# Kernel tuning notes

Measured on AMD Instinct MI355X. Metric: run time of the kernel, lower is better.

The kernel has to match this reference:

```python
import jax, jax.numpy as jnp
import numpy as np

B, V, S, D, H, OBS = 8, 6, 32, 128, 128, 768
LN_EPS = 1e-5
KL_EPS = 1e-5


def setup_inputs() -> dict:
    key = jax.random.key(0)
    ks = jax.random.split(key, 32)
    n = lambda k, sh, s=1.0: jax.random.normal(k, sh, jnp.float32) * s
    w = 0.02  # param init scale
    inp = {
        'student_f0': n(ks[0], (B, V, 256, 32, 88)),
        'student_f1': n(ks[1], (B, V, 512, 16, 44)),
        'teacher_f0': n(ks[2], (B, V, 256, 32, 88)),
        'teacher_f1': n(ks[3], (B, V, 512, 16, 44)),
        'cam_mask': jax.random.randint(ks[4], (B, V), 0, 2).astype(bool),
        'eps_prior': n(ks[5], (V, B, S)),
        'eps_post': n(ks[6], (V, B, S)),
        # obs_encoder: Linear(768,128) -> LN -> SiLU -> Linear(128,128) -> SiLU
        'enc_w1': n(ks[7], (OBS, H), w), 'enc_b1': jnp.zeros((H,)),
        'ln_g': jnp.ones((H,)), 'ln_b': jnp.zeros((H,)),
        'enc_w2': n(ks[8], (H, H), w), 'enc_b2': jnp.zeros((H,)),
        # prior_net: Linear(128,128) -> SiLU -> Linear(128,64)
        'prior_w1': n(ks[9], (D, H), w), 'prior_b1': jnp.zeros((H,)),
        'prior_w2': n(ks[10], (H, 2 * S), w), 'prior_b2': jnp.zeros((2 * S,)),
        # post_net: Linear(128+128,128) -> SiLU -> Linear(128,64)
        'post_w1': n(ks[11], (D + H, H), w), 'post_b1': jnp.zeros((H,)),
        'post_w2': n(ks[12], (H, 2 * S), w), 'post_b2': jnp.zeros((2 * S,)),
        # decoder: Linear(128+32,128) -> SiLU -> Linear(128,768)
        'dec_w1': n(ks[13], (D + S, H), w), 'dec_b1': jnp.zeros((H,)),
        'dec_w2': n(ks[14], (H, OBS), w), 'dec_b2': jnp.zeros((OBS,)),
        # GRUCell(32 -> 128), torch gate order r,z,n
        'gru_wih': n(ks[15], (S, 3 * D), w), 'gru_whh': n(ks[16], (D, 3 * D), w),
        'gru_bih': jnp.zeros((3 * D,)), 'gru_bhh': jnp.zeros((3 * D,)),
    }
    return inp


def _layernorm(x, g, b):
    mu = x.mean(-1, keepdims=True)
    var = ((x - mu) ** 2).mean(-1, keepdims=True)
    return (x - mu) * jax.lax.rsqrt(var + LN_EPS) * g + b


def _rssm(obs, tgt, mask_f, eps_prior, eps_post, p):
    # obs/tgt: [V,B,OBS]; mask_f: [V,B]; eps: [V,B,S]
    silu = jax.nn.silu

    def step(carry, xs):
        deter, rl, rs, kl_acc, kn = carry
        obs_t, tgt_t, m_t, ep_pr, ep_po = xs
        # obs encoder
        h1 = silu(_layernorm(obs_t @ p['enc_w1'] + p['enc_b1'], p['ln_g'], p['ln_b']))
        obs_embed = silu(h1 @ p['enc_w2'] + p['enc_b2'])
        # prior / posterior stats
        pr = silu(deter @ p['prior_w1'] + p['prior_b1']) @ p['prior_w2'] + p['prior_b2']
        prior_mu, prior_lv = pr[..., :S], pr[..., S:]
        po_in = jnp.concatenate([deter, obs_embed], axis=-1)
        po = silu(po_in @ p['post_w1'] + p['post_b1']) @ p['post_w2'] + p['post_b2']
        post_mu, post_lv = po[..., :S], po[..., S:]
        # reparameterize both, select prior where camera is missing
        z_post = post_mu + ep_po * jnp.exp(0.5 * post_lv)
        z_prior = prior_mu + ep_pr * jnp.exp(0.5 * prior_lv)
        m = m_t[:, None]  # [B,1] float, 1 = use prior
        z = jnp.where(m > 0, z_prior, z_post)
        # GRUCell
        gi = z @ p['gru_wih'] + p['gru_bih']
        gh = deter @ p['gru_whh'] + p['gru_bhh']
        ir, iz, inn = jnp.split(gi, 3, axis=-1)
        hr, hz, hn = jnp.split(gh, 3, axis=-1)
        r = jax.nn.sigmoid(ir + hr)
        u = jax.nn.sigmoid(iz + hz)
        nn_ = jnp.tanh(inn + r * hn)
        deter = (1.0 - u) * nn_ + u * deter
        # decoder + losses
        decoded = silu(jnp.concatenate([deter, z], axis=-1) @ p['dec_w1'] + p['dec_b1']) @ p['dec_w2'] + p['dec_b2']
        recon = ((decoded - tgt_t) ** 2).mean(-1, keepdims=True)  # [B,1]
        miss_sum = m.sum()
        has_rec = miss_sum > 0
        rl = rl + jnp.where(has_rec, (recon * m).sum() / jnp.maximum(miss_sum, 1.0), 0.0)
        rs = rs + has_rec.astype(jnp.float32)
        var_q = jnp.maximum(jnp.exp(post_lv), KL_EPS)
        var_p = jnp.maximum(jnp.exp(prior_lv), KL_EPS)
        kl = 0.5 * ((var_q + (post_mu - prior_mu) ** 2) / var_p - 1.0 + prior_lv - post_lv)
        kl = kl.sum(-1, keepdims=True)  # [B,1]
        obs_m = 1.0 - m
        obs_sum = obs_m.sum()
        has_kl = obs_sum > 0
        kl_acc = kl_acc + jnp.where(has_kl, (kl * obs_m).sum() / jnp.maximum(obs_sum, 1.0), 0.0)
        kn = kn + has_kl.astype(jnp.float32)
        return (deter, rl, rs, kl_acc, kn), None

    init = (jnp.zeros((obs.shape[1], D), obs.dtype), 0.0, 0.0, 0.0, 0.0)
    (deter, rl, rs, kl_acc, kn), _ = jax.lax.scan(step, init, (obs, tgt, mask_f, eps_prior, eps_post))
    rec_loss = rl / jnp.maximum(rs, 1.0)
    kl_loss = kl_acc / jnp.maximum(kn, 1.0)
    return rec_loss, kl_loss


def reference(student_f0, student_f1, teacher_f0, teacher_f1, cam_mask, eps_prior, eps_post,
              enc_w1, enc_b1, ln_g, ln_b, enc_w2, enc_b2,
              prior_w1, prior_b1, prior_w2, prior_b2,
              post_w1, post_b1, post_w2, post_b2,
              dec_w1, dec_b1, dec_w2, dec_b2,
              gru_wih, gru_whh, gru_bih, gru_bhh):
    p = dict(enc_w1=enc_w1, enc_b1=enc_b1, ln_g=ln_g, ln_b=ln_b, enc_w2=enc_w2, enc_b2=enc_b2,
             prior_w1=prior_w1, prior_b1=prior_b1, prior_w2=prior_w2, prior_b2=prior_b2,
             post_w1=post_w1, post_b1=post_b1, post_w2=post_w2, post_b2=post_b2,
             dec_w1=dec_w1, dec_b1=dec_b1, dec_w2=dec_w2, dec_b2=dec_b2,
             gru_wih=gru_wih, gru_whh=gru_whh, gru_bih=gru_bih, gru_bhh=gru_bhh)
    # multi-scale spatial mean-pool then concat channels: [B,V,OBS]
    obs = jnp.concatenate([student_f0.mean((-1, -2)), student_f1.mean((-1, -2))], axis=-1)
    tgt = jax.lax.stop_gradient(
        jnp.concatenate([teacher_f0.mean((-1, -2)), teacher_f1.mean((-1, -2))], axis=-1))
    obs_T = jnp.transpose(obs, (1, 0, 2))   # [V,B,OBS]
    tgt_T = jnp.transpose(tgt, (1, 0, 2))
    mask_T = cam_mask.astype(jnp.float32).T  # [V,B]
    rec_loss, kl_loss = _rssm(obs_T, tgt_T, mask_T, eps_prior, eps_post, p)
    return jnp.stack([rec_loss * 1.0, kl_loss * 1e-4])  # [loss_world_rec, loss_world_kl]
```

## Files before the change

### kernel.cpp

```cpp
#include <hip/hip_runtime.h>
#include <cstddef>

constexpr int NB = 8;
constexpr int NV = 6;
constexpr int NS = 32;
constexpr int ND = 128;
constexpr int NH = 128;
constexpr int NOBS = 768;

constexpr int NJOBS = 18432;
constexpr int RWAVES = 8192;

typedef float vf4 __attribute__((ext_vector_type(4)));

__device__ __forceinline__ float sigf(float x) { return 1.0f / (1.0f + expf(-x)); }
__device__ __forceinline__ float siluf(float x) { return x / (1.0f + expf(-x)); }

__device__ __forceinline__ const vf4* lndr(const void* p) {
    asm volatile("" : "+s"(p));
    return (const vf4*)p;
}
#define PHASE_FENCE() do { __builtin_amdgcn_sched_barrier(0); asm volatile("" ::: "memory"); } while (0)

template<int NB8>
__device__ __forceinline__ vf4 dotk(const vf4* __restrict__ w, int ldg, int g, int k0,
                                    const float* __restrict__ x) {
    vf4 acc = {0.f, 0.f, 0.f, 0.f};
    vf4 wa[8], wb[8];
    #pragma unroll
    for (int i = 0; i < 8; i++) wa[i] = w[(size_t)(k0 + i) * ldg + g];
    #pragma unroll
    for (int bb = 0; bb < NB8; bb++) {
        int kb = k0 + bb * 8;
        if ((bb & 1) == 0) {
            if (bb + 1 < NB8) {
                #pragma unroll
                for (int i = 0; i < 8; i++) wb[i] = w[(size_t)(kb + 8 + i) * ldg + g];
            }
            #pragma unroll
            for (int i = 0; i < 8; i++) acc += x[kb + i] * wa[i];
        } else {
            if (bb + 1 < NB8) {
                #pragma unroll
                for (int i = 0; i < 8; i++) wa[i] = w[(size_t)(kb + 8 + i) * ldg + g];
            }
            #pragma unroll
            for (int i = 0; i < 8; i++) acc += x[kb + i] * wb[i];
        }
    }
    return acc;
}

__device__ __forceinline__ void reduce_job(int wid, int lane,
    const float* __restrict__ f0, const float* __restrict__ f1,
    float* __restrict__ out)
{
    if (wid < 12288) {
        const vf4* s4 = (const vf4*)(f0 + (size_t)wid * 2816);
        vf4 xb[11];
        #pragma unroll
        for (int it = 0; it < 11; it++) xb[it] = __builtin_nontemporal_load(&s4[lane + it * 64]);
        float s = 0.f;
        #pragma unroll
        for (int it = 0; it < 11; it++) s += xb[it].x + xb[it].y + xb[it].z + xb[it].w;
        #pragma unroll
        for (int o = 32; o > 0; o >>= 1) s += __shfl_down(s, o);
        if (lane == 0) {
            int b = wid / 1536, r = wid % 1536, v = r >> 8, c = r & 255;
            out[(size_t)(v * NB + b) * NOBS + c] = s * (1.0f / 2816.0f);
        }
    } else {
        int q = wid - 12288;
        int g = lane >> 4, sub = lane & 15;
        const vf4* s4 = (const vf4*)(f1 + (size_t)q * 2816);
        vf4 xb[11];
        #pragma unroll
        for (int it = 0; it < 11; it++) xb[it] = __builtin_nontemporal_load(&s4[g * 176 + sub + it * 16]);
        float s = 0.f;
        #pragma unroll
        for (int it = 0; it < 11; it++) s += xb[it].x + xb[it].y + xb[it].z + xb[it].w;
        #pragma unroll
        for (int o = 8; o > 0; o >>= 1) s += __shfl_down(s, o, 16);
        if (sub == 0) {
            int c4 = 4 * q + g;
            int b = c4 / 3072, r = c4 % 3072, v = r >> 9, c = r & 511;
            out[(size_t)(v * NB + b) * NOBS + 256 + c] = s * (1.0f / 704.0f);
        }
    }
}

__global__ __launch_bounds__(256) void reduce_obs(
    const float* __restrict__ sf0, const float* __restrict__ sf1,
    float* __restrict__ obs)
{
    int lane = threadIdx.x & 63;
    int w0 = blockIdx.x * 4 + (threadIdx.x >> 6);
    for (int wid = w0; wid < NJOBS; wid += RWAVES)
        reduce_job(wid, lane, sf0, sf1, obs);
}

__global__ __launch_bounds__(512) void encoder(
    const float* __restrict__ obs,
    const float* __restrict__ w1, const float* __restrict__ b1,
    const float* __restrict__ g, const float* __restrict__ be,
    const float* __restrict__ w2, const float* __restrict__ b2,
    float* __restrict__ obs_embed,
    const void* cam, float* __restrict__ maskf,
    const float* __restrict__ prior_w1, const float* __restrict__ post_w1,
    const float* __restrict__ prior_w2, const float* __restrict__ post_w2,
    const float* __restrict__ gru_wih,  const float* __restrict__ gru_whh,
    float* __restrict__ warm_dummy)
{
    int tid = threadIdx.x;

    if (blockIdx.x == 48) {
        if (tid != 0) return;
        const int* wi = (const int*)cam;
        bool is_i32 = true;
        for (int i = 0; i < NB * NV; i++) {
            unsigned v = (unsigned)wi[i];
            if (v > 1u) { is_i32 = false; break; }
        }
        const unsigned char* wb = (const unsigned char*)cam;
        for (int b = 0; b < NB; b++)
            for (int v = 0; v < NV; v++) {
                int val = is_i32 ? wi[b * NV + v] : (int)wb[b * NV + v];
                maskf[v * NB + b] = val ? 1.0f : 0.0f;
            }
        return;
    }
    if (blockIdx.x > 48) {
        int wtid = (blockIdx.x - 49) * 512 + tid;
        const float* arrs[6] = {prior_w1, post_w1, prior_w2, post_w2, gru_wih, gru_whh};
        const int n4s[6] = {4096, 8192, 2048, 2048, 3072, 12288};
        float s = 0.f;
        for (int a = 0; a < 6; a++) {
            const vf4* p = (const vf4*)arrs[a];
            int n4 = n4s[a];
            for (int i = wtid; i < n4; i += 16 * 512) {
                vf4 x = p[i];
                s += x.x + x.y + x.z + x.w;
            }
        }
        warm_dummy[wtid & 63] = s;
        return;
    }

    __shared__ float xs[NOBS];
    __shared__ float hs[NH];
    __shared__ float pE[4][NH];
    __shared__ float red[2], red2[2];
    int r = blockIdx.x;
    const float* row = obs + (size_t)r * NOBS;
    for (int i = tid; i < NOBS; i += 512) xs[i] = row[i];
    __syncthreads();

    {
        int part = tid >> 7, j = tid & 127;
        int k0 = part * 192;
        float a = 0.0f;
        #pragma unroll 8
        for (int k = k0; k < k0 + 192; k++) a += xs[k] * w1[k * NH + j];
        pE[part][j] = a;
    }
    __syncthreads();

    float a1 = 0.0f;
    if (tid < NH) {
        a1 = b1[tid] + pE[0][tid] + pE[1][tid] + pE[2][tid] + pE[3][tid];
        float v = a1;
        for (int o = 32; o > 0; o >>= 1) v += __shfl_down(v, o);
        if ((tid & 63) == 0) red[tid >> 6] = v;
    }
    __syncthreads();
    if (tid < NH) {
        float mu = (red[0] + red[1]) * (1.0f / 128.0f);
        float d = a1 - mu;
        float dv = d * d;
        for (int o = 32; o > 0; o >>= 1) dv += __shfl_down(dv, o);
        if ((tid & 63) == 0) red2[tid >> 6] = dv;
    }
    __syncthreads();
    if (tid < NH) {
        float mu = (red[0] + red[1]) * (1.0f / 128.0f);
        float var = (red2[0] + red2[1]) * (1.0f / 128.0f);
        float xn = (a1 - mu) * rsqrtf(var + 1e-5f) * g[tid] + be[tid];
        hs[tid] = siluf(xn);
    }
    __syncthreads();

    {
        int part = tid >> 7, j = tid & 127;
        int k0 = part * 32;
        float a = 0.0f;
        #pragma unroll 8
        for (int k = k0; k < k0 + 32; k++) a += hs[k] * w2[k * NH + j];
        pE[part][j] = a;
    }
    __syncthreads();
    if (tid < NH) {
        float a = b2[tid] + pE[0][tid] + pE[1][tid] + pE[2][tid] + pE[3][tid];
        obs_embed[(size_t)r * NH + tid] = siluf(a);
    }
}

__global__ __launch_bounds__(256) void fused_scan_tgt(
    const float* __restrict__ obs_embed,
    const float* __restrict__ maskf,
    const float* __restrict__ eps_prior, const float* __restrict__ eps_post,
    const float* __restrict__ prior_w1, const float* __restrict__ prior_b1,
    const float* __restrict__ prior_w2, const float* __restrict__ prior_b2,
    const float* __restrict__ post_w1, const float* __restrict__ post_b1,
    const float* __restrict__ post_w2, const float* __restrict__ post_b2,
    const float* __restrict__ gru_wih, const float* __restrict__ gru_whh,
    const float* __restrict__ gru_bih, const float* __restrict__ gru_bhh,
    float* __restrict__ deter_all, float* __restrict__ z_all,
    float* __restrict__ kl_out,
    const float* __restrict__ tf0, const float* __restrict__ tf1,
    float* __restrict__ tgt)
{
    __shared__ float pbuf[1024];
    __shared__ float gi_s[3 * ND];
    __shared__ float deter_obs[ND + NH];
    __shared__ float t12[2 * NH];
    __shared__ float pmu[NS], plv[NS], qmu[NS], qlv[NS], zsm[NS];
    vf4* pbuf4 = (vf4*)pbuf;
    float* deter = deter_obs;

    int tid = threadIdx.x;

    if (blockIdx.x >= 8) {
        int lane = tid & 63;
        int w0 = (blockIdx.x - 8) * 4 + (tid >> 6);
        for (int wid = w0; wid < NJOBS; wid += RWAVES)
            reduce_job(wid, lane, tf0, tf1, tgt);
        return;
    }

    int b = blockIdx.x;

    if (tid < ND) deter[tid] = 0.0f;
    __syncthreads();

    for (int t = 0; t < NV; t++) {
        const vf4* w_pw1  = lndr(prior_w1);
        const vf4* w_ow1  = lndr(post_w1);
        const vf4* w_pw2  = lndr(prior_w2);
        const vf4* w_ow2  = lndr(post_w2);
        const vf4* w_gih  = lndr(gru_wih);
        const vf4* w_ghh  = lndr(gru_whh);

        int rb = t * NB + b;
        if (tid < NH) deter_obs[ND + tid] = obs_embed[(size_t)rb * NH + tid];
        __syncthreads();
        PHASE_FENCE();

        if (tid < 128) {
            int g = tid & 31, part = tid >> 5;
            vf4 acc = dotk<4>(w_pw1, 32, g, part * 32, deter);
            pbuf4[part * 32 + g] = acc;
        } else {
            int u = tid - 128;
            int g = u & 31, part = u >> 5;
            vf4 acc = dotk<8>(w_ow1, 32, g, part * 64, deter_obs);
            pbuf4[128 + part * 32 + g] = acc;
        }
        __syncthreads();
        PHASE_FENCE();
        {
            int j = tid;
            float a = 0.0f;
            if (j < NH) {
                int g = j >> 2, c = j & 3;
                #pragma unroll
                for (int p = 0; p < 4; p++) a += pbuf[(p * 32 + g) * 4 + c];
                t12[j] = siluf(a + prior_b1[j]);
            } else {
                int jj = j - NH;
                int g = jj >> 2, c = jj & 3;
                #pragma unroll
                for (int p = 0; p < 4; p++) a += pbuf[(128 + p * 32 + g) * 4 + c];
                t12[NH + jj] = siluf(a + post_b1[jj]);
            }
        }
        __syncthreads();
        PHASE_FENCE();

        {
            bool isPrior = tid < 128;
            int u = isPrior ? tid : tid - 128;
            int g = u & 15, part = u >> 4;
            const vf4* w = isPrior ? w_pw2 : w_ow2;
            const float* act = t12 + (isPrior ? 0 : NH);
            vf4 acc = dotk<2>(w, 16, g, part * 16, act);
            pbuf4[(isPrior ? 0 : 128) + part * 16 + g] = acc;
        }
        __syncthreads();
        PHASE_FENCE();
        if (tid < 128) {
            int j = tid;
            float a = 0.0f;
            if (j < 64) {
                int g = j >> 2, c = j & 3;
                #pragma unroll
                for (int p = 0; p < 8; p++) a += pbuf[(p * 16 + g) * 4 + c];
                a += prior_b2[j];
                if (j < NS) pmu[j] = a; else plv[j - NS] = a;
            } else {
                int jj = j - 64;
                int g = jj >> 2, c = jj & 3;
                #pragma unroll
                for (int p = 0; p < 8; p++) a += pbuf[(128 + p * 16 + g) * 4 + c];
                a += post_b2[jj];
                if (jj < NS) qmu[jj] = a; else qlv[jj - NS] = a;
            }
        }
        __syncthreads();
        PHASE_FENCE();

        if (tid < NS) {
            float m = maskf[rb];
            float zp = pmu[tid] + eps_prior[(size_t)rb * NS + tid] * expf(0.5f * plv[tid]);
            float zq = qmu[tid] + eps_post[(size_t)rb * NS + tid] * expf(0.5f * qlv[tid]);
            float z = (m > 0.0f) ? zp : zq;
            zsm[tid] = z;
            z_all[(size_t)rb * NS + tid] = z;
            float vq = fmaxf(expf(qlv[tid]), 1e-5f);
            float vp = fmaxf(expf(plv[tid]), 1e-5f);
            float dm = qmu[tid] - pmu[tid];
            float kle = 0.5f * ((vq + dm * dm) / vp - 1.0f + plv[tid] - qlv[tid]);
            for (int o = 16; o > 0; o >>= 1) kle += __shfl_down(kle, o, 32);
            if (tid == 0) kl_out[rb] = kle;
        }
        __syncthreads();
        PHASE_FENCE();

        if (tid < 64) {
            vf4 acc = dotk<4>(w_gih, 96, tid, 0, zsm);
            gi_s[4 * tid + 0] = acc.x + gru_bih[4 * tid + 0];
            gi_s[4 * tid + 1] = acc.y + gru_bih[4 * tid + 1];
            gi_s[4 * tid + 2] = acc.z + gru_bih[4 * tid + 2];
            gi_s[4 * tid + 3] = acc.w + gru_bih[4 * tid + 3];
            if (tid < 32) {
                int g2 = 64 + tid;
                vf4 a2 = dotk<4>(w_gih, 96, g2, 0, zsm);
                gi_s[4 * g2 + 0] = a2.x + gru_bih[4 * g2 + 0];
                gi_s[4 * g2 + 1] = a2.y + gru_bih[4 * g2 + 1];
                gi_s[4 * g2 + 2] = a2.z + gru_bih[4 * g2 + 2];
                gi_s[4 * g2 + 3] = a2.w + gru_bih[4 * g2 + 3];
            }
        } else {
            int u = tid - 64;
            int g = u % 96, part = u / 96;
            vf4 acc = dotk<8>(w_ghh, 96, g, part * 64, deter);
            pbuf4[part * 96 + g] = acc;
        }
        __syncthreads();
        PHASE_FENCE();

        if (tid < ND) {
            int j = tid;
            int gr = j >> 2, c = j & 3;
            float hr = gru_bhh[j]          + pbuf[(gr) * 4 + c]      + pbuf[(96 + gr) * 4 + c];
            float hz = gru_bhh[ND + j]     + pbuf[(32 + gr) * 4 + c] + pbuf[(96 + 32 + gr) * 4 + c];
            float hn = gru_bhh[2 * ND + j] + pbuf[(64 + gr) * 4 + c] + pbuf[(96 + 64 + gr) * 4 + c];
            float r = sigf(gi_s[j] + hr);
            float u = sigf(gi_s[ND + j] + hz);
            float n = tanhf(gi_s[2 * ND + j] + r * hn);
            float dn = (1.0f - u) * n + u * deter[j];
            deter[j] = dn;
            deter_all[(size_t)rb * ND + j] = dn;
        }
        __syncthreads();
        PHASE_FENCE();
    }
}

__global__ __launch_bounds__(512) void decoder_kernel(
    const float* __restrict__ deter_all, const float* __restrict__ z_all,
    const float* __restrict__ tgt,
    const float* __restrict__ dec_w1, const float* __restrict__ dec_b1,
    const float* __restrict__ dec_w2, const float* __restrict__ dec_b2,
    float* __restrict__ recon_out)
{
    int rb = blockIdx.x;
    int tid = threadIdx.x;
    __shared__ float din[ND + NS];
    __shared__ float d1[NH];
    __shared__ float p1[4][NH];
    __shared__ float redb[8];

    if (tid < ND) din[tid] = deter_all[(size_t)rb * ND + tid];
    else if (tid < ND + NS) din[tid] = z_all[(size_t)rb * NS + (tid - ND)];
    __syncthreads();

    {
        int part = tid >> 7, j = tid & 127;
        int k0 = part * 40;
        float a = 0.0f;
        #pragma unroll 8
        for (int k = k0; k < k0 + 40; k++) a += din[k] * dec_w1[k * NH + j];
        p1[part][j] = a;
    }
    __syncthreads();
    if (tid < NH) {
        float a = dec_b1[tid] + p1[0][tid] + p1[1][tid] + p1[2][tid] + p1[3][tid];
        d1[tid] = siluf(a);
    }
    __syncthreads();

    float se = 0.0f;
    const float* trow = tgt + (size_t)rb * NOBS;
    for (int o = tid; o < NOBS; o += 512) {
        float a = dec_b2[o];
        #pragma unroll 8
        for (int i = 0; i < NH; i++) a += d1[i] * dec_w2[i * NOBS + o];
        float df = a - trow[o];
        se += df * df;
    }
    for (int o = 32; o > 0; o >>= 1) se += __shfl_down(se, o);
    if ((tid & 63) == 0) redb[tid >> 6] = se;
    __syncthreads();
    if (tid == 0) {
        float s = 0.0f;
        for (int p = 0; p < 8; p++) s += redb[p];
        recon_out[rb] = s * (1.0f / 768.0f);
    }
}

__global__ void finalize(const float* __restrict__ maskf,
                         const float* __restrict__ recon,
                         const float* __restrict__ kl,
                         float* __restrict__ out)
{
    if (threadIdx.x != 0 || blockIdx.x != 0) return;
    float rl = 0.0f, rs = 0.0f, ka = 0.0f, kn = 0.0f;
    for (int t = 0; t < NV; t++) {
        float ms = 0.0f, rsum = 0.0f, osum = 0.0f, ksum = 0.0f;
        for (int b = 0; b < NB; b++) {
            float m = maskf[t * NB + b];
            ms += m;
            rsum += recon[t * NB + b] * m;
            osum += 1.0f - m;
            ksum += kl[t * NB + b] * (1.0f - m);
        }
        if (ms > 0.0f) { rl += rsum / fmaxf(ms, 1.0f); rs += 1.0f; }
        if (osum > 0.0f) { ka += ksum / fmaxf(osum, 1.0f); kn += 1.0f; }
    }
    out[0] = rl / fmaxf(rs, 1.0f);
    out[1] = (ka / fmaxf(kn, 1.0f)) * 1e-4f;
}

extern "C" void kernel_launch(void* const* d_in, const int* in_sizes, int n_in,
                              void* d_out, int out_size, void* d_ws, size_t ws_size,
                              hipStream_t stream) {
    const float* sf0 = (const float*)d_in[0];
    const float* sf1 = (const float*)d_in[1];
    const float* tf0 = (const float*)d_in[2];
    const float* tf1 = (const float*)d_in[3];
    const void*  cam = d_in[4];
    const float* eps_prior = (const float*)d_in[5];
    const float* eps_post  = (const float*)d_in[6];
    const float* enc_w1 = (const float*)d_in[7];
    const float* enc_b1 = (const float*)d_in[8];
    const float* ln_g   = (const float*)d_in[9];
    const float* ln_b   = (const float*)d_in[10];
    const float* enc_w2 = (const float*)d_in[11];
    const float* enc_b2 = (const float*)d_in[12];
    const float* prior_w1 = (const float*)d_in[13];
    const float* prior_b1 = (const float*)d_in[14];
    const float* prior_w2 = (const float*)d_in[15];
    const float* prior_b2 = (const float*)d_in[16];
    const float* post_w1 = (const float*)d_in[17];
    const float* post_b1 = (const float*)d_in[18];
    const float* post_w2 = (const float*)d_in[19];
    const float* post_b2 = (const float*)d_in[20];
    const float* dec_w1 = (const float*)d_in[21];
    const float* dec_b1 = (const float*)d_in[22];
    const float* dec_w2 = (const float*)d_in[23];
    const float* dec_b2 = (const float*)d_in[24];
    const float* gru_wih = (const float*)d_in[25];
    const float* gru_whh = (const float*)d_in[26];
    const float* gru_bih = (const float*)d_in[27];
    const float* gru_bhh = (const float*)d_in[28];

    float* ws = (float*)d_ws;
    float* obs   = ws;
    float* tgt   = ws + 36864;
    float* oe    = ws + 73728;
    float* maskf = ws + 79872;
    float* rec   = ws + 79920;
    float* klv   = ws + 79968;
    float* deter_all = ws + 80016;
    float* z_all     = ws + 86160;
    float* warm_dummy = ws + 87696;

    reduce_obs<<<RWAVES / 4, 256, 0, stream>>>(sf0, sf1, obs);
    encoder<<<65, 512, 0, stream>>>(obs, enc_w1, enc_b1, ln_g, ln_b, enc_w2, enc_b2, oe,
                                    cam, maskf,
                                    prior_w1, post_w1, prior_w2, post_w2, gru_wih, gru_whh,
                                    warm_dummy);
    fused_scan_tgt<<<8 + RWAVES / 4, 256, 0, stream>>>(
                                     oe, maskf, eps_prior, eps_post,
                                     prior_w1, prior_b1, prior_w2, prior_b2,
                                     post_w1, post_b1, post_w2, post_b2,
                                     gru_wih, gru_whh, gru_bih, gru_bhh,
                                     deter_all, z_all, klv,
                                     tf0, tf1, tgt);
    decoder_kernel<<<48, 512, 0, stream>>>(deter_all, z_all, tgt,
                                           dec_w1, dec_b1, dec_w2, dec_b2, rec);
    finalize<<<1, 64, 0, stream>>>(maskf, rec, klv, (float*)d_out);
}
```

Baseline: 98.29 us.

## Shorten RSSM scan critical path and fold finalize into decoder via atomic counter

Restructures the per-step serial scan. The hidden-to-hidden GRU matvec now runs alongside the first-layer prior/post matvecs, which use full-K dot products instead of split-K partial sums, and the mean/logvar reduction is merged into the KL/sampling stage. Together these remove several __syncthreads barriers per timestep, and the next step's obs embedding is prefetched during the GRU update. The separate finalize launch is removed: the last decoder block to finish, detected with an atomic counter reset in the encoder, computes the final losses. The cost is less thread parallelism per phase, since only a few threads do long dot products, plus a dependence on threadfence/atomic ordering.

```diff
diff --git a/kernel.cpp b/kernel.cpp
--- a/kernel.cpp
+++ b/kernel.cpp
@@ -105,7 +105,7 @@
     const float* __restrict__ g, const float* __restrict__ be,
     const float* __restrict__ w2, const float* __restrict__ b2,
     float* __restrict__ obs_embed,
-    const void* cam, float* __restrict__ maskf,
+    const void* cam, float* __restrict__ maskf, int* __restrict__ done_cnt,
     const float* __restrict__ prior_w1, const float* __restrict__ post_w1,
     const float* __restrict__ prior_w2, const float* __restrict__ post_w2,
     const float* __restrict__ gru_wih,  const float* __restrict__ gru_whh,
@@ -115,6 +115,7 @@
 
     if (blockIdx.x == 48) {
         if (tid != 0) return;
+        *done_cnt = 0;
         const int* wi = (const int*)cam;
         bool is_i32 = true;
         for (int i = 0; i < NB * NV; i++) {
@@ -221,9 +222,10 @@
 {
     __shared__ float pbuf[1024];
     __shared__ float gi_s[3 * ND];
+    __shared__ float ghs[3 * ND];
     __shared__ float deter_obs[ND + NH];
     __shared__ float t12[2 * NH];
-    __shared__ float pmu[NS], plv[NS], qmu[NS], qlv[NS], zsm[NS];
+    __shared__ float zsm[NS];
     vf4* pbuf4 = (vf4*)pbuf;
     float* deter = deter_obs;
 
@@ -240,48 +242,40 @@
     int b = blockIdx.x;
 
     if (tid < ND) deter[tid] = 0.0f;
-    __syncthreads();
+    else deter_obs[ND + (tid - 128)] = obs_embed[(size_t)b * NH + (tid - 128)];
+    __syncthreads();
+    PHASE_FENCE();
 
     for (int t = 0; t < NV; t++) {
-        const vf4* w_pw1  = lndr(prior_w1);
-        const vf4* w_ow1  = lndr(post_w1);
-        const vf4* w_pw2  = lndr(prior_w2);
-        const vf4* w_ow2  = lndr(post_w2);
-        const vf4* w_gih  = lndr(gru_wih);
-        const vf4* w_ghh  = lndr(gru_whh);
+        const vf4* w_pw1 = lndr(prior_w1);
+        const vf4* w_ow1 = lndr(post_w1);
+        const vf4* w_pw2 = lndr(prior_w2);
+        const vf4* w_ow2 = lndr(post_w2);
+        const vf4* w_gih = lndr(gru_wih);
+        const vf4* w_ghh = lndr(gru_whh);
 
         int rb = t * NB + b;
-        if (tid < NH) deter_obs[ND + tid] = obs_embed[(size_t)rb * NH + tid];
-        __syncthreads();
-        PHASE_FENCE();
-
-        if (tid < 128) {
-            int g = tid & 31, part = tid >> 5;
-            vf4 acc = dotk<4>(w_pw1, 32, g, part * 32, deter);
-            pbuf4[part * 32 + g] = acc;
-        } else {
-            int u = tid - 128;
-            int g = u & 31, part = u >> 5;
-            vf4 acc = dotk<8>(w_ow1, 32, g, part * 64, deter_obs);
-            pbuf4[128 + part * 32 + g] = acc;
-        }
-        __syncthreads();
-        PHASE_FENCE();
-        {
-            int j = tid;
-            float a = 0.0f;
-            if (j < NH) {
-                int g = j >> 2, c = j & 3;
-                #pragma unroll
-                for (int p = 0; p < 4; p++) a += pbuf[(p * 32 + g) * 4 + c];
-                t12[j] = siluf(a + prior_b1[j]);
-            } else {
-                int jj = j - NH;
-                int g = jj >> 2, c = jj & 3;
-                #pragma unroll
-                for (int p = 0; p < 4; p++) a += pbuf[(128 + p * 32 + g) * 4 + c];
-                t12[NH + jj] = siluf(a + post_b1[jj]);
-            }
+
+        if (tid < 32) {
+            vf4 acc = dotk<16>(w_pw1, 32, tid, 0, deter);
+            t12[4 * tid + 0] = siluf(acc.x + prior_b1[4 * tid + 0]);
+            t12[4 * tid + 1] = siluf(acc.y + prior_b1[4 * tid + 1]);
+            t12[4 * tid + 2] = siluf(acc.z + prior_b1[4 * tid + 2]);
+            t12[4 * tid + 3] = siluf(acc.w + prior_b1[4 * tid + 3]);
+        } else if (tid < 128) {
+            int g = tid - 32;
+            vf4 acc = dotk<16>(w_ghh, 96, g, 0, deter);
+            ghs[4 * g + 0] = acc.x;
+            ghs[4 * g + 1] = acc.y;
+            ghs[4 * g + 2] = acc.z;
+            ghs[4 * g + 3] = acc.w;
+        } else if (tid < 160) {
+            int g = tid - 128;
+            vf4 acc = dotk<32>(w_ow1, 32, g, 0, deter_obs);
+            t12[NH + 4 * g + 0] = siluf(acc.x + post_b1[4 * g + 0]);
+            t12[NH + 4 * g + 1] = siluf(acc.y + post_b1[4 * g + 1]);
+            t12[NH + 4 * g + 2] = siluf(acc.z + post_b1[4 * g + 2]);
+            t12[NH + 4 * g + 3] = siluf(acc.w + post_b1[4 * g + 3]);
         }
         __syncthreads();
         PHASE_FENCE();
@@ -297,79 +291,58 @@
         }
         __syncthreads();
         PHASE_FENCE();
-        if (tid < 128) {
-            int j = tid;
-            float a = 0.0f;
-            if (j < 64) {
-                int g = j >> 2, c = j & 3;
-                #pragma unroll
-                for (int p = 0; p < 8; p++) a += pbuf[(p * 16 + g) * 4 + c];
-                a += prior_b2[j];
-                if (j < NS) pmu[j] = a; else plv[j - NS] = a;
-            } else {
-                int jj = j - 64;
-                int g = jj >> 2, c = jj & 3;
-                #pragma unroll
-                for (int p = 0; p < 8; p++) a += pbuf[(128 + p * 16 + g) * 4 + c];
-                a += post_b2[jj];
-                if (jj < NS) qmu[jj] = a; else qlv[jj - NS] = a;
-            }
-        }
-        __syncthreads();
-        PHASE_FENCE();
 
         if (tid < NS) {
+            int gq = tid >> 2, c = tid & 3;
+            float pm = prior_b2[tid], pl = prior_b2[tid + 32];
+            float qm = post_b2[tid],  ql = post_b2[tid + 32];
+            #pragma unroll
+            for (int p = 0; p < 8; p++) {
+                pm += pbuf[(p * 16 + gq) * 4 + c];
+                pl += pbuf[(p * 16 + 8 + gq) * 4 + c];
+                qm += pbuf[(128 + p * 16 + gq) * 4 + c];
+                ql += pbuf[(128 + p * 16 + 8 + gq) * 4 + c];
+            }
             float m = maskf[rb];
-            float zp = pmu[tid] + eps_prior[(size_t)rb * NS + tid] * expf(0.5f * plv[tid]);
-            float zq = qmu[tid] + eps_post[(size_t)rb * NS + tid] * expf(0.5f * qlv[tid]);
+            float zp = pm + eps_prior[(size_t)rb * NS + tid] * expf(0.5f * pl);
+            float zq = qm + eps_post[(size_t)rb * NS + tid] * expf(0.5f * ql);
             float z = (m > 0.0f) ? zp : zq;
             zsm[tid] = z;
             z_all[(size_t)rb * NS + tid] = z;
-            float vq = fmaxf(expf(qlv[tid]), 1e-5f);
-            float vp = fmaxf(expf(plv[tid]), 1e-5f);
-            float dm = qmu[tid] - pmu[tid];
-            float kle = 0.5f * ((vq + dm * dm) / vp - 1.0f + plv[tid] - qlv[tid]);
+            float vq = fmaxf(expf(ql), 1e-5f);
+            float vp = fmaxf(expf(pl), 1e-5f);
+            float dm = qm - pm;
+            float kle = 0.5f * ((vq + dm * dm) / vp - 1.0f + pl - ql);
             for (int o = 16; o > 0; o >>= 1) kle += __shfl_down(kle, o, 32);
             if (tid == 0) kl_out[rb] = kle;
         }
         __syncthreads();
         PHASE_FENCE();
 
-        if (tid < 64) {
+        if (tid < 96) {
             vf4 acc = dotk<4>(w_gih, 96, tid, 0, zsm);
             gi_s[4 * tid + 0] = acc.x + gru_bih[4 * tid + 0];
             gi_s[4 * tid + 1] = acc.y + gru_bih[4 * tid + 1];
             gi_s[4 * tid + 2] = acc.z + gru_bih[4 * tid + 2];
             gi_s[4 * tid + 3] = acc.w + gru_bih[4 * tid + 3];
-            if (tid < 32) {
-                int g2 = 64 + tid;
-                vf4 a2 = dotk<4>(w_gih, 96, g2, 0, zsm);
-                gi_s[4 * g2 + 0] = a2.x + gru_bih[4 * g2 + 0];
-                gi_s[4 * g2 + 1] = a2.y + gru_bih[4 * g2 + 1];
-                gi_s[4 * g2 + 2] = a2.z + gru_bih[4 * g2 + 2];
-                gi_s[4 * g2 + 3] = a2.w + gru_bih[4 * g2 + 3];
-            }
-        } else {
-            int u = tid - 64;
-            int g = u % 96, part = u / 96;
-            vf4 acc = dotk<8>(w_ghh, 96, g, part * 64, deter);
-            pbuf4[part * 96 + g] = acc;
         }
         __syncthreads();
         PHASE_FENCE();
 
         if (tid < ND) {
             int j = tid;
-            int gr = j >> 2, c = j & 3;
-            float hr = gru_bhh[j]          + pbuf[(gr) * 4 + c]      + pbuf[(96 + gr) * 4 + c];
-            float hz = gru_bhh[ND + j]     + pbuf[(32 + gr) * 4 + c] + pbuf[(96 + 32 + gr) * 4 + c];
-            float hn = gru_bhh[2 * ND + j] + pbuf[(64 + gr) * 4 + c] + pbuf[(96 + 64 + gr) * 4 + c];
+            float hr = ghs[j]          + gru_bhh[j];
+            float hz = ghs[ND + j]     + gru_bhh[ND + j];
+            float hn = ghs[2 * ND + j] + gru_bhh[2 * ND + j];
             float r = sigf(gi_s[j] + hr);
             float u = sigf(gi_s[ND + j] + hz);
             float n = tanhf(gi_s[2 * ND + j] + r * hn);
             float dn = (1.0f - u) * n + u * deter[j];
             deter[j] = dn;
             deter_all[(size_t)rb * ND + j] = dn;
+        } else if (t + 1 < NV) {
+            int j = tid - 128;
+            deter_obs[ND + j] = obs_embed[(size_t)((t + 1) * NB + b) * NH + j];
         }
         __syncthreads();
         PHASE_FENCE();
@@ -381,7 +354,9 @@
     const float* __restrict__ tgt,
     const float* __restrict__ dec_w1, const float* __restrict__ dec_b1,
     const float* __restrict__ dec_w2, const float* __restrict__ dec_b2,
-    float* __restrict__ recon_out)
+    float* __restrict__ recon_out,
+    const float* __restrict__ maskf, const float* __restrict__ kl,
+    int* __restrict__ done_cnt, float* __restrict__ out)
 {
     int rb = blockIdx.x;
     int tid = threadIdx.x;
@@ -425,30 +400,27 @@
         float s = 0.0f;
         for (int p = 0; p < 8; p++) s += redb[p];
         recon_out[rb] = s * (1.0f / 768.0f);
-    }
-}
-
-__global__ void finalize(const float* __restrict__ maskf,
-                         const float* __restrict__ recon,
-                         const float* __restrict__ kl,
-                         float* __restrict__ out)
-{
-    if (threadIdx.x != 0 || blockIdx.x != 0) return;
-    float rl = 0.0f, rs = 0.0f, ka = 0.0f, kn = 0.0f;
-    for (int t = 0; t < NV; t++) {
-        float ms = 0.0f, rsum = 0.0f, osum = 0.0f, ksum = 0.0f;
-        for (int b = 0; b < NB; b++) {
-            float m = maskf[t * NB + b];
-            ms += m;
-            rsum += recon[t * NB + b] * m;
-            osum += 1.0f - m;
-            ksum += kl[t * NB + b] * (1.0f - m);
-        }
-        if (ms > 0.0f) { rl += rsum / fmaxf(ms, 1.0f); rs += 1.0f; }
-        if (osum > 0.0f) { ka += ksum / fmaxf(osum, 1.0f); kn += 1.0f; }
-    }
-    out[0] = rl / fmaxf(rs, 1.0f);
-    out[1] = (ka / fmaxf(kn, 1.0f)) * 1e-4f;
+        __threadfence();
+        int old = atomicAdd(done_cnt, 1);
+        if (old == 47) {
+            __threadfence();
+            float rl = 0.0f, rs = 0.0f, ka = 0.0f, kn = 0.0f;
+            for (int t = 0; t < NV; t++) {
+                float ms = 0.0f, rsum = 0.0f, osum = 0.0f, ksum = 0.0f;
+                for (int bb = 0; bb < NB; bb++) {
+                    float m = maskf[t * NB + bb];
+                    ms += m;
+                    rsum += recon_out[t * NB + bb] * m;
+                    osum += 1.0f - m;
+                    ksum += kl[t * NB + bb] * (1.0f - m);
+                }
+                if (ms > 0.0f) { rl += rsum / fmaxf(ms, 1.0f); rs += 1.0f; }
+                if (osum > 0.0f) { ka += ksum / fmaxf(osum, 1.0f); kn += 1.0f; }
+            }
+            out[0] = rl / fmaxf(rs, 1.0f);
+            out[1] = (ka / fmaxf(kn, 1.0f)) * 1e-4f;
+        }
+    }
 }
 
 extern "C" void kernel_launch(void* const* d_in, const int* in_sizes, int n_in,
@@ -494,10 +466,11 @@
     float* deter_all = ws + 80016;
     float* z_all     = ws + 86160;
     float* warm_dummy = ws + 87696;
+    int*   done_cnt   = (int*)(ws + 87760);
 
     reduce_obs<<<RWAVES / 4, 256, 0, stream>>>(sf0, sf1, obs);
     encoder<<<65, 512, 0, stream>>>(obs, enc_w1, enc_b1, ln_g, ln_b, enc_w2, enc_b2, oe,
-                                    cam, maskf,
+                                    cam, maskf, done_cnt,
                                     prior_w1, post_w1, prior_w2, post_w2, gru_wih, gru_whh,
                                     warm_dummy);
     fused_scan_tgt<<<8 + RWAVES / 4, 256, 0, stream>>>(
@@ -508,6 +481,6 @@
                                      deter_all, z_all, klv,
                                      tf0, tf1, tgt);
     decoder_kernel<<<48, 512, 0, stream>>>(deter_all, z_all, tgt,
-                                           dec_w1, dec_b1, dec_w2, dec_b2, rec);
-    finalize<<<1, 64, 0, stream>>>(maskf, rec, klv, (float*)d_out);
-}
+                                           dec_w1, dec_b1, dec_w2, dec_b2, rec,
+                                           maskf, klv, done_cnt, (float*)d_out);
+}
```

New measurement: 109.7 us. +11.6%, slower.
